# Optimization experiments

Hardware: AMD Instinct MI355X
Metric: run time of the kernel (lower is better)

The kernel has to match this reference:

```python
import jax, jax.numpy as jnp
import numpy as np

B, N, D = 8, 1024, 768
NHEAD = 4
N_EDGES = 3
ITERS = 2
DK = D // NHEAD


def setup_inputs() -> dict:
    key = jax.random.key(0)
    ks = jax.random.split(key, 12)
    s = 0.02
    return {
        "nodes_embed": jax.random.normal(ks[0], (B, N, D), dtype=jnp.float32),
        "node_adj": jax.random.randint(ks[1], (B, N, N), 0, 4, dtype=jnp.int32),
        # per-edge-type Q/K linear layers (torch Linear: y = x W^T + b; stored here as [in,out])
        "Wq": jax.random.normal(ks[2], (N_EDGES, D, D), dtype=jnp.float32) * s,
        "bq": jax.random.normal(ks[3], (N_EDGES, D), dtype=jnp.float32) * s,
        "Wk": jax.random.normal(ks[4], (N_EDGES, D, D), dtype=jnp.float32) * s,
        "bk": jax.random.normal(ks[5], (N_EDGES, D), dtype=jnp.float32) * s,
        # GCN weights: shared across heads (self.blocks reuses the same Sequential), distinct per iter
        "gcn_W": jax.random.normal(ks[6], (ITERS, D, D), dtype=jnp.float32) * s,
        "gcn_b": jnp.zeros((ITERS, D), dtype=jnp.float32),
        # aggregate_W: Linear(D*nhead -> D), stored as [D*nhead, D]
        "W_agg": jax.random.normal(ks[7], (D * NHEAD, D), dtype=jnp.float32) * s,
        "b_agg": jnp.zeros((D,), dtype=jnp.float32),
    }


def reference(nodes_embed, node_adj, Wq, bq, Wk, bk, gcn_W, gcn_b, W_agg, b_agg):
    Bv, Nv, Dv = nodes_embed.shape
    h, dk = NHEAD, DK
    adj = node_adj[:, None, :, :]  # [B,1,N,N]
    scale = 1.0 / jnp.sqrt(jnp.asarray(dk, nodes_embed.dtype))

    scores = jnp.zeros((Bv, h, Nv, Nv), dtype=nodes_embed.dtype)
    for e in range(N_EDGES):  # small fixed edge-type loop
        q = (nodes_embed @ Wq[e] + bq[e]).reshape(Bv, Nv, h, dk).transpose(0, 2, 1, 3)  # [B,h,N,dk]
        k = (nodes_embed @ Wk[e] + bk[e]).reshape(Bv, Nv, h, dk).transpose(0, 2, 1, 3)
        s = jnp.einsum('bhnd,bhmd->bhnm', q, k) * scale
        scores = scores + jnp.where(adj == e + 1, s, jnp.zeros((), s.dtype))
    scores = jnp.where(scores == 0, jnp.asarray(-1e9, scores.dtype), scores)
    attn = jax.nn.softmax(scores, axis=-1)          # [B,h,N,N]
    ga = jnp.transpose(attn, (1, 0, 2, 3))          # [h,B,N,N]

    # GCN blocks, vectorized over heads; weights shared across heads
    X = jnp.broadcast_to(nodes_embed, (h, Bv, Nv, Dv))  # [h,B,N,D]
    for i in range(ITERS):
        H = jnp.einsum('hbnd,de->hbne', X, gcn_W[i])
        sum_nei = jnp.einsum('hbnm,hbmd->hbnd', ga, H)
        degs = jnp.sum(ga, axis=-1, keepdims=True)       # [h,B,N,1]
        dst = sum_nei / degs + gcn_b[i]
        X = X + jax.nn.relu(dst)

    # torch.cat over heads along feature dim -> [B,N,h*D]
    cat = jnp.transpose(X, (1, 2, 0, 3)).reshape(Bv, Nv, h * Dv)
    out = cat @ W_agg + b_agg
    return out, ga
```

## Files before the change

### kernel.cpp

```cpp
#include <hip/hip_runtime.h>

typedef long long i64;
typedef unsigned short u16;
typedef __attribute__((ext_vector_type(8))) short short8;
typedef __attribute__((ext_vector_type(4))) float f32x4;

#define Bv 8
#define Nv 1024
#define Dv 768
#define Hh 4
#define DKv 192
#define BND ((i64)Bv * Nv * Dv)
#define HBND ((i64)Hh * BND)

__device__ __forceinline__ u16 f2bf(float f) {
    unsigned u = __builtin_bit_cast(unsigned, f);
    u += 0x7fffu + ((u >> 16) & 1u);
    return (u16)(u >> 16);
}
__device__ __forceinline__ float bf2f(u16 h) {
    unsigned u = ((unsigned)h) << 16;
    return __builtin_bit_cast(float, u);
}

__device__ __forceinline__ void gl_lds16(const u16* g, u16* l) {
    __builtin_amdgcn_global_load_lds(
        (const __attribute__((address_space(1))) void*)g,
        (__attribute__((address_space(3))) void*)l, 16, 0, 0);
}

template <int EPI, bool CATK, int ORD, int NBN, int NBM, int NZ>
__global__ __launch_bounds__(256) void gemm_bf16(
    const u16* __restrict__ A, i64 sA, int lda,
    const u16* __restrict__ Bt, i64 sBt, int ldbt, int zmaskBt,
    const float* __restrict__ bias, i64 sBias, const float* __restrict__ bias2,
    void* __restrict__ Cv, i64 sC, int ldc, int K, int koff)
{
    __shared__ u16 Asb[128 * 64];
    __shared__ u16 Bsb[128 * 64];

    const int L = (blockIdx.x & 7) * ((NBN * NBM * NZ) >> 3) + (blockIdx.x >> 3);
    int bn, bm, z;
    if (ORD == 0) {
        bn = L % NBN; const int t2 = L / NBN; bm = t2 % NBM; z = t2 / NBM;
    } else {
        bn = L % NBN; const int t2 = L / NBN; z = t2 % NZ; bm = t2 / NZ;
    }

    A  += (i64)z * sA;
    Bt += (i64)(z & zmaskBt) * sBt;
    const float* bp = bias;
    int zb = z;
    if (bias2 != nullptr && z >= NZ / 2) { bp = bias2; zb = z - NZ / 2; }
    if (bp) bp += (i64)zb * sBias;
    const int kb = z * koff;

    const int bmp = bm * 128, bnp = bn * 128;
    const int tid = threadIdx.x;
    const int w = tid >> 6, l = tid & 63;
    const int wr = w >> 1, wc = w & 1;
    const int kgrp = l >> 4, lr = l & 15;

    const u16* Ab = A + (i64)bmp * lda;
    const u16* Bb = Bt + (i64)bnp * ldbt;

    f32x4 acc[4][4];
    #pragma unroll
    for (int i = 0; i < 4; ++i)
        #pragma unroll
        for (int j = 0; j < 4; ++j)
            acc[i][j] = (f32x4){0.f, 0.f, 0.f, 0.f};

    for (int k0i = 0; k0i < K; k0i += 64) {
        const int k0 = kb + k0i;
        if (k0i) __syncthreads();
        #pragma unroll
        for (int t = 0; t < 4; ++t) {
            const int idx = t * 256 + tid;
            const int r = idx >> 3, s = idx & 7;
            const int ss = s ^ (r & 7);
            const u16* src;
            if (CATK) {
                src = A + (i64)(k0 / Dv) * BND + (i64)(bmp + r) * Dv + (k0 % Dv) + ss * 8;
            } else {
                src = Ab + (i64)r * lda + k0 + ss * 8;
            }
            gl_lds16(src, &Asb[(t * 256 + w * 64) * 8]);
        }
        #pragma unroll
        for (int t = 0; t < 4; ++t) {
            const int idx = t * 256 + tid;
            const int r = idx >> 3, s = idx & 7;
            const int ss = s ^ (r & 7);
            gl_lds16(Bb + (i64)r * ldbt + k0 + ss * 8, &Bsb[(t * 256 + w * 64) * 8]);
        }
        __syncthreads();

        #pragma unroll
        for (int ks = 0; ks < 2; ++ks) {
            const int slot = ks * 4 + kgrp;
            short8 a[4], b[4];
            #pragma unroll
            for (int i = 0; i < 4; ++i) {
                const int r = wc * 64 + i * 16 + lr;
                a[i] = *(const short8*)&Bsb[r * 64 + ((slot ^ (r & 7)) << 3)];
            }
            #pragma unroll
            for (int j = 0; j < 4; ++j) {
                const int r = wr * 64 + j * 16 + lr;
                b[j] = *(const short8*)&Asb[r * 64 + ((slot ^ (r & 7)) << 3)];
            }
            #pragma unroll
            for (int i = 0; i < 4; ++i)
                #pragma unroll
                for (int j = 0; j < 4; ++j)
                    acc[i][j] = __builtin_amdgcn_mfma_f32_16x16x32_bf16(
                        a[i], b[j], acc[i][j], 0, 0, 0);
        }
    }

    f32x4 bj[4];
    #pragma unroll
    for (int i = 0; i < 4; ++i) {
        const int nb = bnp + wc * 64 + i * 16 + kgrp * 4;
        bj[i] = bp ? *(const f32x4*)&bp[nb] : (f32x4){0.f, 0.f, 0.f, 0.f};
    }

    #pragma unroll
    for (int j = 0; j < 4; ++j) {
        const int m = bmp + wr * 64 + j * 16 + lr;
        #pragma unroll
        for (int i = 0; i < 4; ++i) {
            const int nb = bnp + wc * 64 + i * 16 + kgrp * 4;
            const i64 off = (i64)z * sC + (i64)m * ldc + nb;
            f32x4 v = acc[i][j] + bj[i];
            if (EPI == 0) {
                *(f32x4*)&((float*)Cv)[off] = v;
            } else if (EPI == 1) {
                ushort4 o;
                o.x = f2bf(v[0]); o.y = f2bf(v[1]);
                o.z = f2bf(v[2]); o.w = f2bf(v[3]);
                *(ushort4*)&((u16*)Cv)[off] = o;
            } else {
                u16* xp = (u16*)Cv + off;
                ushort4 old = *(const ushort4*)xp;
                ushort4 o;
                o.x = f2bf(bf2f(old.x) + fmaxf(v[0], 0.f));
                o.y = f2bf(bf2f(old.y) + fmaxf(v[1], 0.f));
                o.z = f2bf(bf2f(old.z) + fmaxf(v[2], 0.f));
                o.w = f2bf(bf2f(old.w) + fmaxf(v[3], 0.f));
                *(ushort4*)xp = o;
            }
        }
    }
}

__global__ __launch_bounds__(256) void scores_mfma(
    const u16* __restrict__ qb, const u16* __restrict__ kb,
    const int* __restrict__ adj, u16* __restrict__ sb)
{
    __shared__ u16 Qs[2][64 * 64];
    __shared__ u16 Ks[2][64 * 64];

    const int bid = blockIdx.x;
    const int b = bid & 7;
    const int t2 = bid >> 3;
    const int h = t2 & 3;
    const int mt = (t2 >> 2) & 15;
    const int nt = t2 >> 6;
    const int m0 = mt * 64, n0 = nt * 64;
    const int zga = h * 8 + b;

    const int tid = threadIdx.x;
    const int w = tid >> 6, l = tid & 63;
    const int wr = w >> 1, wc = w & 1;
    const int kgrp = l >> 4, lr = l & 15;

    const i64 qoff = ((i64)b * Nv + n0) * Dv + h * DKv;
    const i64 koff = ((i64)b * Nv + m0) * Dv + h * DKv;

#define STAGE_SC(ci_, buf_) { \
    const int e_ = (ci_) / 3, k0_ = ((ci_) % 3) * 64; \
    const u16* qe_ = qb + (i64)e_ * BND + qoff; \
    const u16* ke_ = kb + (i64)e_ * BND + koff; \
    _Pragma("unroll") \
    for (int t = 0; t < 2; ++t) { \
        const int idx2 = t * 256 + tid; \
        const int r = idx2 >> 3, s = idx2 & 7; \
        const int ss = s ^ (r & 7); \
        gl_lds16(qe_ + (i64)r * Dv + k0_ + ss * 8, &Qs[buf_][(t * 256 + w * 64) * 8]); \
        gl_lds16(ke_ + (i64)r * Dv + k0_ + ss * 8, &Ks[buf_][(t * 256 + w * 64) * 8]); \
    } }

    int4 adjv[2][2];
    #pragma unroll
    for (int i = 0; i < 2; ++i) {
        const int mb = m0 + wc * 32 + i * 16 + kgrp * 4;
        #pragma unroll
        for (int j = 0; j < 2; ++j) {
            const int n = n0 + wr * 32 + j * 16 + lr;
            adjv[i][j] = *(const int4*)&adj[((i64)b * Nv + n) * Nv + mb];
        }
    }

    f32x4 acc[3][2][2];
    #pragma unroll
    for (int e = 0; e < 3; ++e)
        #pragma unroll
        for (int i = 0; i < 2; ++i)
            #pragma unroll
            for (int j = 0; j < 2; ++j)
                acc[e][i][j] = (f32x4){0.f, 0.f, 0.f, 0.f};

    STAGE_SC(0, 0)

    #pragma unroll
    for (int ci = 0; ci < 9; ++ci) {
        const int cur = ci & 1;
        if (ci < 8) {
            if (cur) { STAGE_SC(ci + 1, 0) } else { STAGE_SC(ci + 1, 1) }
            asm volatile("s_waitcnt vmcnt(4)" ::: "memory");
        } else {
            asm volatile("s_waitcnt vmcnt(0)" ::: "memory");
        }
        __builtin_amdgcn_s_barrier();
        asm volatile("" ::: "memory");

        const int e = ci / 3;
        #pragma unroll
        for (int ks = 0; ks < 2; ++ks) {
            const int slot = ks * 4 + kgrp;
            short8 a[2], bq2[2];
            #pragma unroll
            for (int i = 0; i < 2; ++i) {
                const int r = wc * 32 + i * 16 + lr;
                a[i] = *(const short8*)&Ks[cur][r * 64 + ((slot ^ (r & 7)) << 3)];
            }
            #pragma unroll
            for (int j = 0; j < 2; ++j) {
                const int r = wr * 32 + j * 16 + lr;
                bq2[j] = *(const short8*)&Qs[cur][r * 64 + ((slot ^ (r & 7)) << 3)];
            }
            #pragma unroll
            for (int i = 0; i < 2; ++i)
                #pragma unroll
                for (int j = 0; j < 2; ++j)
                    acc[e][i][j] = __builtin_amdgcn_mfma_f32_16x16x32_bf16(
                        a[i], bq2[j], acc[e][i][j], 0, 0, 0);
        }

        asm volatile("s_waitcnt lgkmcnt(0)" ::: "memory");
        __builtin_amdgcn_s_barrier();
    }
#undef STAGE_SC

    const float scale = 0.07216878364870323f;
    #pragma unroll
    for (int i = 0; i < 2; ++i) {
        const int mb = m0 + wc * 32 + i * 16 + kgrp * 4;
        #pragma unroll
        for (int j = 0; j < 2; ++j) {
            const int n = n0 + wr * 32 + j * 16 + lr;
            const int av[4] = {adjv[i][j].x, adjv[i][j].y, adjv[i][j].z, adjv[i][j].w};
            ushort4 o;
            #pragma unroll
            for (int rg = 0; rg < 4; ++rg) {
                float f = 0.f;
                if (av[rg] == 1) f = acc[0][i][j][rg];
                else if (av[rg] == 2) f = acc[1][i][j][rg];
                else if (av[rg] == 3) f = acc[2][i][j][rg];
                f *= scale;
                if (f == 0.f) f = -1e9f;
                ((u16*)&o)[rg] = f2bf(f);
            }
            *(ushort4*)&sb[((i64)zga * Nv + n) * Nv + mb] = o;
        }
    }
}

__global__ __launch_bounds__(256) void softmax_k(const u16* __restrict__ sb,
                                                 float* __restrict__ ga,
                                                 u16* __restrict__ gab)
{
    const i64 row = blockIdx.x;
    const int tid = threadIdx.x;
    const int wid = tid >> 6, lane = tid & 63;

    ushort4 sv = *(const ushort4*)&sb[row * (i64)Nv + tid * 4];
    float4 v;
    v.x = bf2f(sv.x); v.y = bf2f(sv.y); v.z = bf2f(sv.z); v.w = bf2f(sv.w);

    float m = fmaxf(fmaxf(v.x, v.y), fmaxf(v.z, v.w));
    #pragma unroll
    for (int o = 32; o >= 1; o >>= 1) m = fmaxf(m, __shfl_xor(m, o));

    __shared__ float red[4];
    if (lane == 0) red[wid] = m;
    __syncthreads();
    m = fmaxf(fmaxf(red[0], red[1]), fmaxf(red[2], red[3]));

    float e0 = expf(v.x - m), e1 = expf(v.y - m), e2 = expf(v.z - m), e3 = expf(v.w - m);
    float s = e0 + e1 + e2 + e3;
    #pragma unroll
    for (int o = 32; o >= 1; o >>= 1) s += __shfl_xor(s, o);
    __syncthreads();
    if (lane == 0) red[wid] = s;
    __syncthreads();
    s = red[0] + red[1] + red[2] + red[3];

    const float inv = 1.0f / s;
    float4 o;
    o.x = e0 * inv; o.y = e1 * inv; o.z = e2 * inv; o.w = e3 * inv;
    *(float4*)&ga[row * (i64)Nv + tid * 4] = o;

    ushort4 ob;
    ob.x = f2bf(o.x); ob.y = f2bf(o.y); ob.z = f2bf(o.z); ob.w = f2bf(o.w);
    *(ushort4*)&gab[row * (i64)Nv + tid * 4] = ob;
}

__global__ __launch_bounds__(256) void prep_k(const float* __restrict__ nodes,
                                              u16* __restrict__ nodesb,
                                              u16* __restrict__ Xb)
{
    const i64 i = (i64)blockIdx.x * 256 + threadIdx.x;
    float4 v = ((const float4*)nodes)[i];
    ushort4 o;
    o.x = f2bf(v.x); o.y = f2bf(v.y); o.z = f2bf(v.z); o.w = f2bf(v.w);
    ((ushort4*)nodesb)[i] = o;
    const i64 q4 = BND / 4;
    #pragma unroll
    for (int h = 0; h < Hh; ++h) ((ushort4*)Xb)[(i64)h * q4 + i] = o;
}

__global__ __launch_bounds__(256) void trans_all(
    const float* __restrict__ Wq, const float* __restrict__ Wk,
    const float* __restrict__ gcnW, const float* __restrict__ Wagg,
    u16* __restrict__ wqkt, u16* __restrict__ gcnWt, u16* __restrict__ waggt)
{
    const int z = blockIdx.z;
    const i64 W768 = (i64)768 * 768;
    const float* src;
    u16* dst;
    int ldo;
    if (z < 3)      { src = Wq + z * W768;        dst = wqkt + z * W768;          ldo = 768; }
    else if (z < 6) { src = Wk + (z - 3) * W768;  dst = wqkt + (i64)z * W768;     ldo = 768; }
    else if (z < 8) { src = gcnW + (z - 6) * W768; dst = gcnWt + (i64)(z - 6) * W768; ldo = 768; }
    else            { src = Wagg + (i64)(z - 8) * W768; dst = waggt + (i64)(z - 8) * 768; ldo = 3072; }

    __shared__ u16 t[32][33];
    const int c0 = blockIdx.x * 32, r0 = blockIdx.y * 32;
    const int tx = threadIdx.x & 31, ty = threadIdx.x >> 5;
    #pragma unroll
    for (int i = ty; i < 32; i += 8)
        t[i][tx] = f2bf(src[(i64)(r0 + i) * 768 + c0 + tx]);
    __syncthreads();
    #pragma unroll
    for (int i = ty; i < 32; i += 8)
        dst[(i64)(c0 + i) * ldo + r0 + tx] = t[tx][i];
}

__global__ __launch_bounds__(256) void addbias_k(
    const float* __restrict__ p0, const float* __restrict__ p1,
    const float* __restrict__ bias, float* __restrict__ out)
{
    const i64 i4 = (i64)blockIdx.x * 256 + threadIdx.x;
    const int nb = (int)((i4 * 4) % Dv);
    float4 a = ((const float4*)p0)[i4];
    float4 b = ((const float4*)p1)[i4];
    float4 bv = *(const float4*)&bias[nb];
    float4 o;
    o.x = a.x + b.x + bv.x; o.y = a.y + b.y + bv.y;
    o.z = a.z + b.z + bv.z; o.w = a.w + b.w + bv.w;
    ((float4*)out)[i4] = o;
}

extern "C" void kernel_launch(void* const* d_in, const int* in_sizes, int n_in,
                              void* d_out, int out_size, void* d_ws, size_t ws_size,
                              hipStream_t stream)
{
    const float* nodes = (const float*)d_in[0];
    const int*   adj   = (const int*)d_in[1];
    const float* Wq    = (const float*)d_in[2];
    const float* bq    = (const float*)d_in[3];
    const float* Wk    = (const float*)d_in[4];
    const float* bk    = (const float*)d_in[5];
    const float* gcnW  = (const float*)d_in[6];
    const float* gcnb  = (const float*)d_in[7];
    const float* Wagg  = (const float*)d_in[8];
    const float* bagg  = (const float*)d_in[9];

    float* out = (float*)d_out;
    float* gaf = out + BND;

    const i64 W768 = (i64)768 * 768;
    const i64 HTZ  = (i64)768 * 1024;
    u16* ws     = (u16*)d_ws;
    u16* qb     = ws;
    u16* kb2    = ws + 3 * BND;
    u16* gab    = ws;
    u16* nodesb = ws + 6 * BND;
    u16* gcnWt  = nodesb + BND;
    u16* waggt  = gcnWt + 2 * W768;
    u16* Xb     = waggt + 4 * W768;
    u16* Htz    = Xb + HBND;
    u16* wqkt   = Htz;
    u16* sbuf   = Htz;
    float* part = (float*)Htz;

    dim3 blk(256);

    prep_k<<<dim3((unsigned)(BND / 4 / 256)), blk, 0, stream>>>(nodes, nodesb, Xb);
    trans_all<<<dim3(24, 24, 12), blk, 0, stream>>>(Wq, Wk, gcnW, Wagg, wqkt, gcnWt, waggt);

    gemm_bf16<1, false, 1, 6, 64, 6><<<dim3(2304), blk, 0, stream>>>(
        nodesb, 0, Dv, wqkt, W768, Dv, -1, bq, Dv, bk, qb, BND, Dv, Dv, 0);

    scores_mfma<<<dim3(8192), blk, 0, stream>>>(qb, kb2, adj, sbuf);

    softmax_k<<<dim3(Hh * Bv * Nv), blk, 0, stream>>>(sbuf, gaf, gab);

    for (int it = 0; it < 2; ++it) {
        if (it == 0) {
            gemm_bf16<1, false, 0, 8, 6, 8><<<dim3(384), blk, 0, stream>>>(
                gcnWt, 0, Dv, nodesb, (i64)Nv * Dv, Dv, 7, nullptr, 0, nullptr,
                Htz, HTZ, 1024, Dv, 0);
            gemm_bf16<2, false, 0, 6, 8, 32><<<dim3(1536), blk, 0, stream>>>(
                gab, (i64)Nv * Nv, Nv, Htz, HTZ, 1024, 7, gcnb, 0, nullptr,
                Xb, (i64)Nv * Dv, Dv, Nv, 0);
        } else {
            gemm_bf16<1, false, 0, 8, 6, 32><<<dim3(1536), blk, 0, stream>>>(
                gcnWt + W768, 0, Dv, Xb, (i64)Nv * Dv, Dv, 31, nullptr, 0, nullptr,
                Htz, HTZ, 1024, Dv, 0);
            gemm_bf16<2, false, 0, 6, 8, 32><<<dim3(1536), blk, 0, stream>>>(
                gab, (i64)Nv * Nv, Nv, Htz, HTZ, 1024, 31, gcnb + (i64)Dv, 0, nullptr,
                Xb, (i64)Nv * Dv, Dv, Nv, 0);
        }
    }

    gemm_bf16<0, true, 0, 6, 64, 2><<<dim3(768), blk, 0, stream>>>(
        Xb, 0, Dv, waggt, 0, Hh * Dv, -1, nullptr, 0, nullptr,
        part, BND, Dv, (Hh * Dv) / 2, (Hh * Dv) / 2);

    addbias_k<<<dim3((unsigned)(BND / 4 / 256)), blk, 0, stream>>>(
        part, part + BND, bagg, out);
}
```

Baseline: 542.7 us.

## Add triple-buffered 128x256-tile GEMM with 512 threads for GCN matmuls

Adds a new GEMM kernel using 512-thread blocks, 128x256 output tiles and a three-stage LDS ring that prefetches two K-tiles ahead with direct global-to-LDS loads. Uses it for the aggregation GEMMs and the second-iteration weight GEMM in place of the 128x128 double-buffered kernel. The intent is more data reuse per tile and better overlap of global loads with MFMA work. In exchange it uses more LDS and registers per block and halves the grid size, which may lower occupancy.

```diff
diff --git a/kernel.cpp b/kernel.cpp
--- a/kernel.cpp
+++ b/kernel.cpp
@@ -28,6 +28,8 @@
         (const __attribute__((address_space(1))) void*)g,
         (__attribute__((address_space(3))) void*)l, 16, 0, 0);
 }
+
+#define VMCNT(n) asm volatile("s_waitcnt vmcnt(" #n ")" ::: "memory")
 
 template <int EPI, bool CATK, int ORD, int NBN, int NBM, int NZ>
 __global__ __launch_bounds__(256) void gemm_bf16(
@@ -155,6 +157,144 @@
     }
 }
 
+template <int EPI, int NBN, int NBM, int NZ>
+__global__ __launch_bounds__(512, 2) void gemm_tri(
+    const u16* __restrict__ A, i64 sA, int lda,
+    const u16* __restrict__ Bt, i64 sBt, int ldbt, int zmask,
+    const float* __restrict__ bias,
+    u16* __restrict__ Out, i64 sO, int ldo, int K)
+{
+    __shared__ u16 AsbF[3 * 128 * 64];
+    __shared__ u16 BsbF[3 * 256 * 64];
+
+    const int L = (blockIdx.x & 7) * ((NBN * NBM * NZ) >> 3) + (blockIdx.x >> 3);
+    const int bn = L % NBN;
+    const int t2 = L / NBN;
+    const int bm = t2 % NBM;
+    const int z  = t2 / NBM;
+
+    const u16* Ag = A + (i64)z * sA + (i64)(bm * 128) * lda;
+    const u16* Bg = Bt + (i64)(z & zmask) * sBt + (i64)(bn * 256) * ldbt;
+
+    const int tid = threadIdx.x;
+    const int w = tid >> 6, l = tid & 63;
+    const int wr = w >> 2;
+    const int wc = w & 3;
+    const int kgrp = l >> 4, lr = l & 15;
+
+    f32x4 acc[4][4];
+    #pragma unroll
+    for (int f = 0; f < 4; ++f)
+        #pragma unroll
+        for (int g = 0; g < 4; ++g)
+            acc[f][g] = (f32x4){0.f, 0.f, 0.f, 0.f};
+
+#define STG(kt_, bb_) { \
+    _Pragma("unroll") \
+    for (int q = 0; q < 2; ++q) { \
+        const int idx = q * 512 + tid; \
+        const int r = idx >> 3, s = idx & 7; \
+        const int ss = s ^ (r & 7); \
+        gl_lds16(Ag + (i64)r * lda + (kt_) * 64 + ss * 8, \
+                 &AsbF[(bb_) * 8192 + (q * 512 + w * 64) * 8]); \
+    } \
+    _Pragma("unroll") \
+    for (int q = 0; q < 4; ++q) { \
+        const int idx = q * 512 + tid; \
+        const int r = idx >> 3, s = idx & 7; \
+        const int ss = s ^ (r & 7); \
+        gl_lds16(Bg + (i64)r * ldbt + (kt_) * 64 + ss * 8, \
+                 &BsbF[(bb_) * 16384 + (q * 512 + w * 64) * 8]); \
+    } }
+
+    const int NT = K / 64;
+    int cur = 0, b2 = 2;
+
+    STG(0, 0)
+    STG(1, 1)
+    VMCNT(6);
+    __builtin_amdgcn_s_barrier();
+    asm volatile("" ::: "memory");
+
+    for (int kt = 0; kt < NT; ++kt) {
+        const u16* Ac = &AsbF[cur * 8192];
+        const u16* Bc = &BsbF[cur * 16384];
+
+        short8 bfr[4][2];
+        #pragma unroll
+        for (int g = 0; g < 4; ++g)
+            #pragma unroll
+            for (int ks = 0; ks < 2; ++ks) {
+                const int r = wc * 64 + g * 16 + lr;
+                const int slot = ks * 4 + kgrp;
+                bfr[g][ks] = *(const short8*)&Bc[r * 64 + ((slot ^ (r & 7)) << 3)];
+            }
+
+        if (kt < NT - 2) { STG(kt + 2, b2) }
+
+        #pragma unroll
+        for (int p = 0; p < 4; ++p) {
+            short8 afr[2];
+            #pragma unroll
+            for (int ks = 0; ks < 2; ++ks) {
+                const int r = wr * 64 + p * 16 + lr;
+                const int slot = ks * 4 + kgrp;
+                afr[ks] = *(const short8*)&Ac[r * 64 + ((slot ^ (r & 7)) << 3)];
+            }
+            __builtin_amdgcn_s_setprio(1);
+            #pragma unroll
+            for (int g = 0; g < 4; ++g)
+                #pragma unroll
+                for (int ks = 0; ks < 2; ++ks)
+                    acc[p][g] = __builtin_amdgcn_mfma_f32_16x16x32_bf16(
+                        bfr[g][ks], afr[ks], acc[p][g], 0, 0, 0);
+            __builtin_amdgcn_s_setprio(0);
+        }
+
+        if (kt < NT - 2) { VMCNT(6); }
+        else if (kt == NT - 2) { VMCNT(0); }
+        if (kt < NT - 1) {
+            __builtin_amdgcn_s_barrier();
+            asm volatile("" ::: "memory");
+        }
+        cur = (cur == 2) ? 0 : cur + 1;
+        b2  = (b2 == 2) ? 0 : b2 + 1;
+    }
+#undef STG
+
+    f32x4 bj[4];
+    #pragma unroll
+    for (int g = 0; g < 4; ++g) {
+        const int n = bn * 256 + wc * 64 + g * 16 + kgrp * 4;
+        bj[g] = bias ? *(const f32x4*)&bias[n] : (f32x4){0.f, 0.f, 0.f, 0.f};
+    }
+
+    #pragma unroll
+    for (int f = 0; f < 4; ++f) {
+        const int m = bm * 128 + wr * 64 + f * 16 + lr;
+        #pragma unroll
+        for (int g = 0; g < 4; ++g) {
+            const int n = bn * 256 + wc * 64 + g * 16 + kgrp * 4;
+            u16* xp = Out + (i64)z * sO + (i64)m * ldo + n;
+            f32x4 v = acc[f][g] + bj[g];
+            if (EPI == 1) {
+                ushort4 o;
+                o.x = f2bf(v[0]); o.y = f2bf(v[1]);
+                o.z = f2bf(v[2]); o.w = f2bf(v[3]);
+                *(ushort4*)xp = o;
+            } else {
+                ushort4 old = *(const ushort4*)xp;
+                ushort4 o;
+                o.x = f2bf(bf2f(old.x) + fmaxf(v[0], 0.f));
+                o.y = f2bf(bf2f(old.y) + fmaxf(v[1], 0.f));
+                o.z = f2bf(bf2f(old.z) + fmaxf(v[2], 0.f));
+                o.w = f2bf(bf2f(old.w) + fmaxf(v[3], 0.f));
+                *(ushort4*)xp = o;
+            }
+        }
+    }
+}
+
 __global__ __launch_bounds__(256) void scores_mfma(
     const u16* __restrict__ qb, const u16* __restrict__ kb,
     const int* __restrict__ adj, u16* __restrict__ sb)
@@ -219,9 +359,9 @@
         const int cur = ci & 1;
         if (ci < 8) {
             if (cur) { STAGE_SC(ci + 1, 0) } else { STAGE_SC(ci + 1, 1) }
-            asm volatile("s_waitcnt vmcnt(4)" ::: "memory");
+            VMCNT(4);
         } else {
-            asm volatile("s_waitcnt vmcnt(0)" ::: "memory");
+            VMCNT(0);
         }
         __builtin_amdgcn_s_barrier();
         asm volatile("" ::: "memory");
@@ -424,16 +564,16 @@
             gemm_bf16<1, false, 0, 8, 6, 8><<<dim3(384), blk, 0, stream>>>(
                 gcnWt, 0, Dv, nodesb, (i64)Nv * Dv, Dv, 7, nullptr, 0, nullptr,
                 Htz, HTZ, 1024, Dv, 0);
-            gemm_bf16<2, false, 0, 6, 8, 32><<<dim3(1536), blk, 0, stream>>>(
-                gab, (i64)Nv * Nv, Nv, Htz, HTZ, 1024, 7, gcnb, 0, nullptr,
-                Xb, (i64)Nv * Dv, Dv, Nv, 0);
+            gemm_tri<2, 3, 8, 32><<<dim3(768), dim3(512), 0, stream>>>(
+                gab, (i64)Nv * Nv, Nv, Htz, HTZ, 1024, 7, gcnb,
+                Xb, (i64)Nv * Dv, Dv, Nv);
         } else {
-            gemm_bf16<1, false, 0, 8, 6, 32><<<dim3(1536), blk, 0, stream>>>(
-                gcnWt + W768, 0, Dv, Xb, (i64)Nv * Dv, Dv, 31, nullptr, 0, nullptr,
-                Htz, HTZ, 1024, Dv, 0);
-            gemm_bf16<2, false, 0, 6, 8, 32><<<dim3(1536), blk, 0, stream>>>(
-                gab, (i64)Nv * Nv, Nv, Htz, HTZ, 1024, 31, gcnb + (i64)Dv, 0, nullptr,
-                Xb, (i64)Nv * Dv, Dv, Nv, 0);
+            gemm_tri<1, 4, 6, 32><<<dim3(768), dim3(512), 0, stream>>>(
+                gcnWt + W768, 0, Dv, Xb, (i64)Nv * Dv, Dv, 31, nullptr,
+                Htz, HTZ, 1024, Dv);
+            gemm_tri<2, 3, 8, 32><<<dim3(768), dim3(512), 0, stream>>>(
+                gab, (i64)Nv * Nv, Nv, Htz, HTZ, 1024, 31, gcnb + (i64)Dv,
+                Xb, (i64)Nv * Dv, Dv, Nv);
         }
     }
 
```

Measured after the change: 597.4 us. +10.1%, slower.
